# Kernel tuning notes

Hardware: AMD Instinct MI355X
Metric: run time of the kernel (lower is better)

The kernel has to match this reference:

```python
import jax, jax.numpy as jnp
import numpy as np

EPS = 1e-06
N_HEADS = 8


def setup_inputs() -> dict:
    key = jax.random.key(0)
    ks = jax.random.split(key, 9)
    B, M, T, C = 2, 64, 256, 512
    s = 0.02
    return {
        "x": jax.random.normal(ks[0], (B, M, T, C), dtype=jnp.float32),
        "Wq": jax.random.normal(ks[1], (C, C), dtype=jnp.float32) * s,
        "bq": jnp.zeros((C,), dtype=jnp.float32),
        "Wk": jax.random.normal(ks[2], (C, C), dtype=jnp.float32) * s,
        "bk": jnp.zeros((C,), dtype=jnp.float32),
        "Wv": jax.random.normal(ks[3], (C, C), dtype=jnp.float32) * s,
        "bv": jnp.zeros((C,), dtype=jnp.float32),
        "Wp": jax.random.normal(ks[4], (C, C), dtype=jnp.float32) * s,
        "bp": jnp.zeros((C,), dtype=jnp.float32),
    }


def _proj_heads(x, W, b, N, D):
    # nn.Linear: x @ W.T + b, then view(B,M,T,N,D).transpose(2,3) -> [B,M,N,T,D]
    B, M, T, C = x.shape
    y = jnp.einsum('bmtc,dc->bmtd', x, W) + b
    return y.reshape(B, M, T, N, D).transpose(0, 1, 3, 2, 4)


def reference(x, Wq, bq, Wk, bk, Wv, bv, Wp, bp):
    B, M, T, C = x.shape
    N = N_HEADS
    D = C // N
    q = _proj_heads(x, Wq, bq, N, D)  # [B,M,N,T,D]
    k = _proj_heads(x, Wk, bk, N, D)
    v = _proj_heads(x, Wv, bv, N, D)
    # ELU+1 feature map
    q = jax.nn.elu(q) + 1.0
    k = jax.nn.elu(k) + 1.0
    # KtV = k^T @ v : [B,M,N,D,D]
    KtV = jnp.einsum('bmntd,bmnte->bmnde', k, v)
    # Z = 1 / (q @ sum_t k + eps) : [B,M,N,T]
    ksum = jnp.sum(k, axis=-2)  # [B,M,N,D]
    z = 1.0 / (jnp.einsum('bmntd,bmnd->bmnt', q, ksum) + EPS)
    # Original does Z.expand(...,D) @ KtV; since Z is constant over the D axis,
    # this equals z[t] * sum_d KtV[d, e] -- compute that directly (faithful math).
    KtV_colsum = jnp.sum(KtV, axis=-2)  # [B,M,N,D]
    V = z[..., None] * KtV_colsum[..., None, :]  # [B,M,N,T,D]
    V = V.transpose(0, 1, 3, 2, 4).reshape(B, M, T, N * D)
    out = jnp.einsum('bmtc,dc->bmtd', V, Wp) + bp
    return out
```

## Files before the change

### kernel.cpp

```cpp
#include <hip/hip_runtime.h>
#include <hip/hip_bf16.h>

#define BM_ 128
#define T_  256
#define C_  512
#define NH  8
#define DH  64

typedef __bf16 bf16;
typedef __attribute__((ext_vector_type(8))) __bf16 bf16x8;
typedef __attribute__((ext_vector_type(4))) float f32x4;

__device__ __forceinline__ float elu1(float v){ return v > 0.f ? v + 1.f : __expf(v); }

__device__ __forceinline__ unsigned short f2bf(float f){
  unsigned u = __float_as_uint(f);
  u += 0x7fffu + ((u >> 16) & 1u);
  return (unsigned short)(u >> 16);
}

__device__ __forceinline__ float bf2f(unsigned short b){
  return __uint_as_float(((unsigned)b) << 16);
}

#define GLOAD16(gptr, lptr) __builtin_amdgcn_global_load_lds( \
  (const __attribute__((address_space(1))) void*)(gptr), \
  (__attribute__((address_space(3))) void*)(lptr), 16, 0, 0)

__global__ __launch_bounds__(256) void cvt3_kernel(
    const float* __restrict__ a, int na4,
    const float* __restrict__ b, int nb4,
    const float* __restrict__ c, int nc4,
    unsigned short* __restrict__ oa, unsigned short* __restrict__ ob,
    unsigned short* __restrict__ oc)
{
  int i = blockIdx.x * blockDim.x + threadIdx.x;
  int stride = gridDim.x * blockDim.x;
  int total = na4 + nb4 + nc4;
  for (; i < total; i += stride) {
    const float* src; unsigned short* dst; int idx;
    if (i < na4)            { src = a; dst = oa; idx = i; }
    else if (i < na4 + nb4) { src = b; dst = ob; idx = i - na4; }
    else                    { src = c; dst = oc; idx = i - na4 - nb4; }
    float4 v = reinterpret_cast<const float4*>(src)[idx];
    ushort4 o;
    o.x = f2bf(v.x); o.y = f2bf(v.y); o.z = f2bf(v.z); o.w = f2bf(v.w);
    reinterpret_cast<ushort4*>(dst)[idx] = o;
  }
}

template<int MODE>
__global__ __launch_bounds__(256) void gemm_proj(
    const bf16* __restrict__ A, const bf16* __restrict__ Bw,
    const float* __restrict__ bias,
    float* __restrict__ krow, float* __restrict__ ksum4,
    const float* __restrict__ ksum4_in, float* __restrict__ zden)
{
  __shared__ bf16 As[2][128 * 32];
  __shared__ bf16 Bs[2][128 * 32];

  const int tid  = threadIdx.x;
  const int lane = tid & 63;
  const int wid  = tid >> 6;
  const int wm   = wid >> 1, wn = wid & 1;

  const int L  = (blockIdx.x & 7) * 128 + (blockIdx.x >> 3);
  const int tn = L & 3, tm = L >> 2;

  f32x4 acc[4][4];
#pragma unroll
  for (int i = 0; i < 4; i++)
#pragma unroll
    for (int j = 0; j < 4; j++) acc[i][j] = (f32x4){0.f, 0.f, 0.f, 0.f};

  const bf16* Ab = A  + (size_t)(tm * 128) * C_;
  const bf16* Bb = Bw + (size_t)(tn * 128) * C_;

  const int r0 = tid >> 2, r1 = r0 + 64;
  const int sl = (tid & 3) * 8;
  const int fr = lane & 15;
  const int fq = lane >> 4;
  const int fk = fq * 8;

#define STAGE(buf, kc) do { \
    GLOAD16(Ab + (size_t)r0 * C_ + (kc) + sl, As[buf] + r0 * 32 + sl); \
    GLOAD16(Ab + (size_t)r1 * C_ + (kc) + sl, As[buf] + r1 * 32 + sl); \
    GLOAD16(Bb + (size_t)r0 * C_ + (kc) + sl, Bs[buf] + r0 * 32 + sl); \
    GLOAD16(Bb + (size_t)r1 * C_ + (kc) + sl, Bs[buf] + r1 * 32 + sl); \
  } while (0)

  STAGE(0, 0);
  asm volatile("s_waitcnt vmcnt(0)" ::: "memory");
  __syncthreads();

  for (int it = 0; it < 15; ++it) {
    const int cur = it & 1;
    STAGE(cur ^ 1, (it + 1) * 32);
    bf16x8 af[4], bfr[4];
#pragma unroll
    for (int i = 0; i < 4; i++)
      af[i] = *reinterpret_cast<const bf16x8*>(&As[cur][(wm * 64 + i * 16 + fr) * 32 + fk]);
#pragma unroll
    for (int j = 0; j < 4; j++)
      bfr[j] = *reinterpret_cast<const bf16x8*>(&Bs[cur][(wn * 64 + j * 16 + fr) * 32 + fk]);
#pragma unroll
    for (int i = 0; i < 4; i++)
#pragma unroll
      for (int j = 0; j < 4; j++)
        acc[i][j] = __builtin_amdgcn_mfma_f32_16x16x32_bf16(af[i], bfr[j], acc[i][j], 0, 0, 0);
    asm volatile("s_waitcnt vmcnt(0)" ::: "memory");
    __syncthreads();
  }
  {
    bf16x8 af[4], bfr[4];
#pragma unroll
    for (int i = 0; i < 4; i++)
      af[i] = *reinterpret_cast<const bf16x8*>(&As[1][(wm * 64 + i * 16 + fr) * 32 + fk]);
#pragma unroll
    for (int j = 0; j < 4; j++)
      bfr[j] = *reinterpret_cast<const bf16x8*>(&Bs[1][(wn * 64 + j * 16 + fr) * 32 + fk]);
#pragma unroll
    for (int i = 0; i < 4; i++)
#pragma unroll
      for (int j = 0; j < 4; j++)
        acc[i][j] = __builtin_amdgcn_mfma_f32_16x16x32_bf16(af[i], bfr[j], acc[i][j], 0, 0, 0);
  }
#undef STAGE

  const int bm   = tm >> 1;
  const int head = tn * 2 + wn;
  float bj[4];
#pragma unroll
  for (int j = 0; j < 4; j++) bj[j] = bias[tn * 128 + wn * 64 + j * 16 + fr];

  if (MODE == 0) {
    float cs[4] = {0.f, 0.f, 0.f, 0.f};
#pragma unroll
    for (int i = 0; i < 4; i++) {
#pragma unroll
      for (int r = 0; r < 4; r++) {
        float rs = 0.f;
#pragma unroll
        for (int j = 0; j < 4; j++) {
          float v = elu1(acc[i][j][r] + bj[j]);
          rs += v;
          cs[j] += v;
        }
#pragma unroll
        for (int m = 1; m < 16; m <<= 1) rs += __shfl_xor(rs, m);
        if (fr == 0) {
          int grow = tm * 128 + wm * 64 + i * 16 + fq * 4 + r;
          krow[((size_t)bm * NH + head) * T_ + (grow & 255)] = rs;
        }
      }
    }
    const int part = (tm & 1) * 2 + wm;
#pragma unroll
    for (int j = 0; j < 4; j++) {
      cs[j] += __shfl_xor(cs[j], 16);
      cs[j] += __shfl_xor(cs[j], 32);
      if (fq == 0)
        ksum4[((size_t)part * BM_ + bm) * C_ + tn * 128 + wn * 64 + j * 16 + fr] = cs[j];
    }
  } else {
    float ks[4];
#pragma unroll
    for (int j = 0; j < 4; j++) {
      size_t col = (size_t)bm * C_ + tn * 128 + wn * 64 + j * 16 + fr;
      ks[j] = ksum4_in[col] + ksum4_in[(size_t)BM_ * C_ + col]
            + ksum4_in[2 * (size_t)BM_ * C_ + col] + ksum4_in[3 * (size_t)BM_ * C_ + col];
    }
#pragma unroll
    for (int i = 0; i < 4; i++) {
#pragma unroll
      for (int r = 0; r < 4; r++) {
        float zs = 0.f;
#pragma unroll
        for (int j = 0; j < 4; j++) zs = fmaf(elu1(acc[i][j][r] + bj[j]), ks[j], zs);
#pragma unroll
        for (int m = 1; m < 16; m <<= 1) zs += __shfl_xor(zs, m);
        if (fr == 0) {
          int grow = tm * 128 + wm * 64 + i * 16 + fq * 4 + r;
          zden[((size_t)bm * NH + head) * T_ + (grow & 255)] = zs;
        }
      }
    }
  }
}

__global__ __launch_bounds__(256) void xk_kernel(
    const unsigned short* __restrict__ xb, const float* __restrict__ krow,
    float* __restrict__ xk2, float* __restrict__ srow2)
{
  const int bm = blockIdx.x, th = blockIdx.y, tid = threadIdx.x;
  __shared__ float krs[NH * 128];
#pragma unroll
  for (int p = 0; p < 4; p++) {
    int idx = tid + p * 256;
    int n = idx >> 7, t = idx & 127;
    krs[idx] = krow[((size_t)bm * NH + n) * T_ + th * 128 + t];
  }
  __syncthreads();
  float a0[8], a1[8];
#pragma unroll
  for (int n = 0; n < 8; n++) { a0[n] = 0.f; a1[n] = 0.f; }
  const unsigned short* xp = xb + ((size_t)bm * T_ + th * 128) * C_ + tid * 2;
  for (int t = 0; t < 128; t++) {
    ushort2 u = *reinterpret_cast<const ushort2*>(xp + (size_t)t * C_);
    float x0 = bf2f(u.x), x1 = bf2f(u.y);
#pragma unroll
    for (int n = 0; n < 8; n++) {
      float kr = krs[n * 128 + t];
      a0[n] = fmaf(kr, x0, a0[n]);
      a1[n] = fmaf(kr, x1, a1[n]);
    }
  }
#pragma unroll
  for (int n = 0; n < 8; n++)
    *reinterpret_cast<float2*>(&xk2[(((size_t)th * BM_ + bm) * NH + n) * C_ + tid * 2])
        = make_float2(a0[n], a1[n]);
  if (tid < 8) {
    float s = 0.f;
    for (int t = 0; t < 128; t++) s += krs[tid * 128 + t];
    srow2[((size_t)th * BM_ + bm) * NH + tid] = s;
  }
}

__global__ __launch_bounds__(256) void colsum_kernel(
    const float* __restrict__ xk2, const float* __restrict__ srow2,
    const float* __restrict__ Wv, const float* __restrict__ bv,
    float* __restrict__ cs_g)
{
  const int bm0 = blockIdx.x * 8, h = blockIdx.y, tid = threadIdx.x;
  __shared__ float4 xs4[8][128];
#pragma unroll
  for (int p = 0; p < 4; p++) {
    int idx = tid + p * 256;
    int bmr = idx >> 7, c4 = idx & 127;
    float4 u = *reinterpret_cast<const float4*>(
        xk2 + (((size_t)0 * BM_ + bm0 + bmr) * NH + h) * C_ + c4 * 4);
    float4 w = *reinterpret_cast<const float4*>(
        xk2 + (((size_t)1 * BM_ + bm0 + bmr) * NH + h) * C_ + c4 * 4);
    xs4[bmr][c4] = make_float4(u.x + w.x, u.y + w.y, u.z + w.z, u.w + w.w);
  }
  __syncthreads();
  const int e = tid & 63, bs = tid >> 6;
  const float4* wv4 = reinterpret_cast<const float4*>(Wv + (size_t)(h * DH + e) * C_);
  float acc0 = 0.f, acc1 = 0.f;
#pragma unroll 4
  for (int c4 = 0; c4 < 128; c4++) {
    float4 w = wv4[c4];
    float4 a = xs4[bs * 2][c4];
    float4 b = xs4[bs * 2 + 1][c4];
    acc0 += w.x * a.x + w.y * a.y + w.z * a.z + w.w * a.w;
    acc1 += w.x * b.x + w.y * b.y + w.z * b.z + w.w * b.w;
  }
  float bve = bv[h * DH + e];
  int bmA = bm0 + bs * 2, bmB = bmA + 1;
  float sA = srow2[(size_t)bmA * NH + h] + srow2[(size_t)(BM_ + bmA) * NH + h];
  float sB = srow2[(size_t)bmB * NH + h] + srow2[(size_t)(BM_ + bmB) * NH + h];
  cs_g[((size_t)bmA * NH + h) * DH + e] = acc0 + sA * bve;
  cs_g[((size_t)bmB * NH + h) * DH + e] = acc1 + sB * bve;
}

__global__ __launch_bounds__(256) void wbuf_kernel(
    const float* __restrict__ cs_g, const float* __restrict__ Wp,
    float* __restrict__ wbuf)
{
  const int cpt = blockIdx.x, h = blockIdx.y, bm0 = blockIdx.z * 16;
  const int tid = threadIdx.x;
  __shared__ float4 csL4[16][16];
  {
    int bmr = tid >> 4, e4 = tid & 15;
    csL4[bmr][e4] = *reinterpret_cast<const float4*>(
        cs_g + ((size_t)(bm0 + bmr) * NH + h) * DH + e4 * 4);
  }
  __syncthreads();
  const int cp = cpt * 256 + tid;
  float4 wp[16];
  const float4* wpr = reinterpret_cast<const float4*>(Wp + (size_t)cp * C_ + h * DH);
#pragma unroll
  for (int e4 = 0; e4 < 16; e4++) wp[e4] = wpr[e4];
#pragma unroll
  for (int bmr = 0; bmr < 16; bmr++) {
    float acc = 0.f;
#pragma unroll
    for (int e4 = 0; e4 < 16; e4++) {
      float4 c = csL4[bmr][e4];
      acc += wp[e4].x * c.x + wp[e4].y * c.y + wp[e4].z * c.z + wp[e4].w * c.w;
    }
    wbuf[((size_t)(bm0 + bmr) * NH + h) * C_ + cp] = acc;
  }
}

__global__ __launch_bounds__(256) void out_kernel(
    const float* __restrict__ zden, const float* __restrict__ wbuf,
    const float* __restrict__ bp, float* __restrict__ out)
{
  const int bm = blockIdx.x, tt = blockIdx.y, tid = threadIdx.x;
  __shared__ float zs[NH][64];
#pragma unroll
  for (int p = 0; p < 2; p++) {
    int idx = tid + p * 256;
    int n = idx >> 6, t = idx & 63;
    zs[n][t] = 1.f / (zden[((size_t)bm * NH + n) * T_ + tt * 64 + t] + 1e-6f);
  }
  float2 wv[8];
  const int c2 = tid * 2;
#pragma unroll
  for (int n = 0; n < 8; n++)
    wv[n] = *reinterpret_cast<const float2*>(wbuf + ((size_t)bm * NH + n) * C_ + c2);
  float2 bpv = *reinterpret_cast<const float2*>(bp + c2);
  __syncthreads();
  float* ob = out + ((size_t)bm * T_ + tt * 64) * C_;
  for (int t = 0; t < 64; t++) {
    float o0 = bpv.x, o1 = bpv.y;
#pragma unroll
    for (int n = 0; n < 8; n++) { float z = zs[n][t]; o0 = fmaf(z, wv[n].x, o0); o1 = fmaf(z, wv[n].y, o1); }
    *reinterpret_cast<float2*>(ob + (size_t)t * C_ + c2) = make_float2(o0, o1);
  }
}

extern "C" void kernel_launch(void* const* d_in, const int* in_sizes, int n_in,
                              void* d_out, int out_size, void* d_ws, size_t ws_size,
                              hipStream_t stream)
{
  const float* x  = (const float*)d_in[0];
  const float* Wq = (const float*)d_in[1];
  const float* bq = (const float*)d_in[2];
  const float* Wk = (const float*)d_in[3];
  const float* bk = (const float*)d_in[4];
  const float* Wv = (const float*)d_in[5];
  const float* bv = (const float*)d_in[6];
  const float* Wp = (const float*)d_in[7];
  const float* bp = (const float*)d_in[8];
  float* out = (float*)d_out;

  float* ws    = (float*)d_ws;
  float* zden  = ws;
  float* ksum4 = zden + 262144;
  float* krow  = ksum4 + 262144;
  float* srow2 = krow + 262144;
  float* xk2   = srow2 + 2048;
  float* cs    = xk2 + 1048576;
  float* wbuf  = cs + 65536;
  unsigned short* xb  = (unsigned short*)(wbuf + 524288);
  unsigned short* wkb = xb + 16777216;
  unsigned short* wqb = wkb + 262144;

  cvt3_kernel<<<2048, 256, 0, stream>>>(x, 16777216 / 4, Wk, 262144 / 4, Wq, 262144 / 4,
                                        xb, wkb, wqb);

  gemm_proj<0><<<1024, 256, 0, stream>>>((const bf16*)xb, (const bf16*)wkb, bk,
                                         krow, ksum4, nullptr, nullptr);
  xk_kernel<<<dim3(BM_, 2), 256, 0, stream>>>(xb, krow, xk2, srow2);
  colsum_kernel<<<dim3(16, 8), 256, 0, stream>>>(xk2, srow2, Wv, bv, cs);
  wbuf_kernel<<<dim3(2, 8, 8), 256, 0, stream>>>(cs, Wp, wbuf);
  gemm_proj<1><<<1024, 256, 0, stream>>>((const bf16*)xb, (const bf16*)wqb, bq,
                                         nullptr, nullptr, ksum4, zden);
  out_kernel<<<dim3(BM_, 4), 256, 0, stream>>>(zden, wbuf, bp, out);
}
```

Before: 135.6 us.

## Enlarge projection GEMM tiles to 256x256 with swizzled LDS and interleaved prefetch

Rewrites the bf16 projection GEMM to use 256x256 block tiles with K=64 steps, 512 threads (8 waves), an XOR-swizzled LDS layout, and prefetch of the next K tile split into chunks between quarter-step MFMA groups, with s_setprio around the MFMA bursts. Larger tiles cut the number of times A and B are re-read from global memory, and the swizzle is meant to avoid LDS bank conflicts. The xk reduction is also split across four T-quarters instead of two to add parallelism. The cost is 128KB of LDS per block and a heavy register footprint, which limits occupancy. The grid also shrinks to 256 blocks, which may leave some CUs unevenly loaded.

```diff
diff --git a/kernel.cpp b/kernel.cpp
--- a/kernel.cpp
+++ b/kernel.cpp
@@ -26,6 +26,8 @@
 #define GLOAD16(gptr, lptr) __builtin_amdgcn_global_load_lds( \
   (const __attribute__((address_space(1))) void*)(gptr), \
   (__attribute__((address_space(3))) void*)(lptr), 16, 0, 0)
+
+#define FENCE() asm volatile("" ::: "memory")
 
 __global__ __launch_bounds__(256) void cvt3_kernel(
     const float* __restrict__ a, int na4,
@@ -50,138 +52,190 @@
 }
 
 template<int MODE>
-__global__ __launch_bounds__(256) void gemm_proj(
+__global__ __launch_bounds__(512, 2) void gemm_proj(
     const bf16* __restrict__ A, const bf16* __restrict__ Bw,
     const float* __restrict__ bias,
-    float* __restrict__ krow, float* __restrict__ ksum4,
-    const float* __restrict__ ksum4_in, float* __restrict__ zden)
-{
-  __shared__ bf16 As[2][128 * 32];
-  __shared__ bf16 Bs[2][128 * 32];
+    float* __restrict__ krow, float* __restrict__ ksum2,
+    const float* __restrict__ ksum2_in, float* __restrict__ zden)
+{
+  __shared__ bf16 As[2][256 * 64];
+  __shared__ bf16 Bs[2][256 * 64];
 
   const int tid  = threadIdx.x;
   const int lane = tid & 63;
   const int wid  = tid >> 6;
-  const int wm   = wid >> 1, wn = wid & 1;
-
-  const int L  = (blockIdx.x & 7) * 128 + (blockIdx.x >> 3);
-  const int tn = L & 3, tm = L >> 2;
-
-  f32x4 acc[4][4];
-#pragma unroll
-  for (int i = 0; i < 4; i++)
-#pragma unroll
-    for (int j = 0; j < 4; j++) acc[i][j] = (f32x4){0.f, 0.f, 0.f, 0.f};
-
-  const bf16* Ab = A  + (size_t)(tm * 128) * C_;
-  const bf16* Bb = Bw + (size_t)(tn * 128) * C_;
-
-  const int r0 = tid >> 2, r1 = r0 + 64;
-  const int sl = (tid & 3) * 8;
-  const int fr = lane & 15;
-  const int fq = lane >> 4;
-  const int fk = fq * 8;
-
-#define STAGE(buf, kc) do { \
-    GLOAD16(Ab + (size_t)r0 * C_ + (kc) + sl, As[buf] + r0 * 32 + sl); \
-    GLOAD16(Ab + (size_t)r1 * C_ + (kc) + sl, As[buf] + r1 * 32 + sl); \
-    GLOAD16(Bb + (size_t)r0 * C_ + (kc) + sl, Bs[buf] + r0 * 32 + sl); \
-    GLOAD16(Bb + (size_t)r1 * C_ + (kc) + sl, Bs[buf] + r1 * 32 + sl); \
-  } while (0)
-
-  STAGE(0, 0);
+  const int wr   = wid >> 2, wc = wid & 3;
+
+  const int L  = ((blockIdx.x & 7) << 5) + (blockIdx.x >> 3);
+  const int tn = L & 1, tm = L >> 1;
+
+  const bf16* Ab = A  + (size_t)(tm * 256) * C_;
+  const bf16* Bb = Bw + (size_t)(tn * 256) * C_;
+
+  const int srow  = tid >> 3;
+  const int sslot = tid & 7;
+  const int fr = lane & 15, fq = lane >> 4;
+
+  f32x4 acc[8][4];
+#pragma unroll
+  for (int m = 0; m < 8; ++m)
+#pragma unroll
+    for (int n = 0; n < 4; ++n) acc[m][n] = (f32x4){0.f, 0.f, 0.f, 0.f};
+
+#define STG(XS, Xb, b, h, kt) do { \
+  _Pragma("unroll") \
+  for (int q = 0; q < 2; ++q) { \
+    int r_ = (h) * 128 + q * 64 + srow; \
+    GLOAD16(Xb + (size_t)r_ * C_ + (kt) * 64 + ((sslot ^ (r_ & 7)) << 3), \
+            &XS[b][(((h) * 128 + q * 64) << 6) + (tid << 3)]); \
+  } } while (0)
+
+#define LOFF(row, sl) (((row) << 6) + ((((sl) ^ ((row) & 7))) << 3))
+
+  STG(As, Ab, 0, 0, 0); STG(As, Ab, 0, 1, 0);
+  STG(Bs, Bb, 0, 0, 0); STG(Bs, Bb, 0, 1, 0);
   asm volatile("s_waitcnt vmcnt(0)" ::: "memory");
-  __syncthreads();
-
-  for (int it = 0; it < 15; ++it) {
-    const int cur = it & 1;
-    STAGE(cur ^ 1, (it + 1) * 32);
-    bf16x8 af[4], bfr[4];
-#pragma unroll
-    for (int i = 0; i < 4; i++)
-      af[i] = *reinterpret_cast<const bf16x8*>(&As[cur][(wm * 64 + i * 16 + fr) * 32 + fk]);
-#pragma unroll
-    for (int j = 0; j < 4; j++)
-      bfr[j] = *reinterpret_cast<const bf16x8*>(&Bs[cur][(wn * 64 + j * 16 + fr) * 32 + fk]);
-#pragma unroll
-    for (int i = 0; i < 4; i++)
-#pragma unroll
-      for (int j = 0; j < 4; j++)
-        acc[i][j] = __builtin_amdgcn_mfma_f32_16x16x32_bf16(af[i], bfr[j], acc[i][j], 0, 0, 0);
+  __builtin_amdgcn_s_barrier();
+  FENCE();
+
+  bf16x8 af[4][2], bfr[4][2];
+
+  for (int t = 0; t < 8; ++t) {
+    const int cur = t & 1;
+    const bool pre = (t < 7);
+#pragma unroll
+    for (int m = 0; m < 4; ++m)
+#pragma unroll
+      for (int kk = 0; kk < 2; ++kk) {
+        int row = wr * 128 + m * 16 + fr;
+        af[m][kk] = *reinterpret_cast<const bf16x8*>(&As[cur][LOFF(row, kk * 4 + fq)]);
+      }
+#pragma unroll
+    for (int n = 0; n < 2; ++n)
+#pragma unroll
+      for (int kk = 0; kk < 2; ++kk) {
+        int row = wc * 64 + n * 16 + fr;
+        bfr[n][kk] = *reinterpret_cast<const bf16x8*>(&Bs[cur][LOFF(row, kk * 4 + fq)]);
+      }
+    if (pre) { STG(As, Ab, cur ^ 1, 0, t + 1); STG(Bs, Bb, cur ^ 1, 0, t + 1); }
+    __builtin_amdgcn_s_setprio(1);
+#pragma unroll
+    for (int m = 0; m < 4; ++m)
+#pragma unroll
+      for (int n = 0; n < 2; ++n)
+#pragma unroll
+        for (int kk = 0; kk < 2; ++kk)
+          acc[m][n] = __builtin_amdgcn_mfma_f32_16x16x32_bf16(af[m][kk], bfr[n][kk], acc[m][n], 0, 0, 0);
+    __builtin_amdgcn_s_setprio(0);
+    __builtin_amdgcn_s_barrier();
+    FENCE();
+#pragma unroll
+    for (int n = 0; n < 2; ++n)
+#pragma unroll
+      for (int kk = 0; kk < 2; ++kk) {
+        int row = wc * 64 + (n + 2) * 16 + fr;
+        bfr[n + 2][kk] = *reinterpret_cast<const bf16x8*>(&Bs[cur][LOFF(row, kk * 4 + fq)]);
+      }
+    if (pre) STG(As, Ab, cur ^ 1, 1, t + 1);
+    __builtin_amdgcn_s_setprio(1);
+#pragma unroll
+    for (int m = 0; m < 4; ++m)
+#pragma unroll
+      for (int n = 0; n < 2; ++n)
+#pragma unroll
+        for (int kk = 0; kk < 2; ++kk)
+          acc[m][n + 2] = __builtin_amdgcn_mfma_f32_16x16x32_bf16(af[m][kk], bfr[n + 2][kk], acc[m][n + 2], 0, 0, 0);
+    __builtin_amdgcn_s_setprio(0);
+    __builtin_amdgcn_s_barrier();
+    FENCE();
+#pragma unroll
+    for (int m = 0; m < 4; ++m)
+#pragma unroll
+      for (int kk = 0; kk < 2; ++kk) {
+        int row = wr * 128 + 64 + m * 16 + fr;
+        af[m][kk] = *reinterpret_cast<const bf16x8*>(&As[cur][LOFF(row, kk * 4 + fq)]);
+      }
+    if (pre) STG(Bs, Bb, cur ^ 1, 1, t + 1);
+    __builtin_amdgcn_s_setprio(1);
+#pragma unroll
+    for (int m = 0; m < 4; ++m)
+#pragma unroll
+      for (int n = 0; n < 2; ++n)
+#pragma unroll
+        for (int kk = 0; kk < 2; ++kk)
+          acc[m + 4][n] = __builtin_amdgcn_mfma_f32_16x16x32_bf16(af[m][kk], bfr[n][kk], acc[m + 4][n], 0, 0, 0);
+    __builtin_amdgcn_s_setprio(0);
+    __builtin_amdgcn_s_barrier();
+    FENCE();
+    __builtin_amdgcn_s_setprio(1);
+#pragma unroll
+    for (int m = 0; m < 4; ++m)
+#pragma unroll
+      for (int n = 0; n < 2; ++n)
+#pragma unroll
+        for (int kk = 0; kk < 2; ++kk)
+          acc[m + 4][n + 2] = __builtin_amdgcn_mfma_f32_16x16x32_bf16(af[m][kk], bfr[n + 2][kk], acc[m + 4][n + 2], 0, 0, 0);
+    __builtin_amdgcn_s_setprio(0);
     asm volatile("s_waitcnt vmcnt(0)" ::: "memory");
-    __syncthreads();
-  }
-  {
-    bf16x8 af[4], bfr[4];
-#pragma unroll
-    for (int i = 0; i < 4; i++)
-      af[i] = *reinterpret_cast<const bf16x8*>(&As[1][(wm * 64 + i * 16 + fr) * 32 + fk]);
-#pragma unroll
-    for (int j = 0; j < 4; j++)
-      bfr[j] = *reinterpret_cast<const bf16x8*>(&Bs[1][(wn * 64 + j * 16 + fr) * 32 + fk]);
-#pragma unroll
-    for (int i = 0; i < 4; i++)
-#pragma unroll
-      for (int j = 0; j < 4; j++)
-        acc[i][j] = __builtin_amdgcn_mfma_f32_16x16x32_bf16(af[i], bfr[j], acc[i][j], 0, 0, 0);
-  }
-#undef STAGE
-
-  const int bm   = tm >> 1;
-  const int head = tn * 2 + wn;
+    __builtin_amdgcn_s_barrier();
+    FENCE();
+  }
+#undef STG
+#undef LOFF
+
+  const int bm   = tm;
+  const int head = tn * 4 + wc;
   float bj[4];
 #pragma unroll
-  for (int j = 0; j < 4; j++) bj[j] = bias[tn * 128 + wn * 64 + j * 16 + fr];
+  for (int n = 0; n < 4; ++n) bj[n] = bias[tn * 256 + wc * 64 + n * 16 + fr];
 
   if (MODE == 0) {
     float cs[4] = {0.f, 0.f, 0.f, 0.f};
 #pragma unroll
-    for (int i = 0; i < 4; i++) {
-#pragma unroll
-      for (int r = 0; r < 4; r++) {
+    for (int m = 0; m < 8; ++m) {
+#pragma unroll
+      for (int r = 0; r < 4; ++r) {
         float rs = 0.f;
 #pragma unroll
-        for (int j = 0; j < 4; j++) {
-          float v = elu1(acc[i][j][r] + bj[j]);
+        for (int n = 0; n < 4; ++n) {
+          float v = elu1(acc[m][n][r] + bj[n]);
           rs += v;
-          cs[j] += v;
+          cs[n] += v;
         }
 #pragma unroll
-        for (int m = 1; m < 16; m <<= 1) rs += __shfl_xor(rs, m);
+        for (int msk = 1; msk < 16; msk <<= 1) rs += __shfl_xor(rs, msk);
         if (fr == 0) {
-          int grow = tm * 128 + wm * 64 + i * 16 + fq * 4 + r;
-          krow[((size_t)bm * NH + head) * T_ + (grow & 255)] = rs;
+          int tg = wr * 128 + m * 16 + fq * 4 + r;
+          krow[((size_t)bm * NH + head) * T_ + tg] = rs;
         }
       }
     }
-    const int part = (tm & 1) * 2 + wm;
-#pragma unroll
-    for (int j = 0; j < 4; j++) {
-      cs[j] += __shfl_xor(cs[j], 16);
-      cs[j] += __shfl_xor(cs[j], 32);
+#pragma unroll
+    for (int n = 0; n < 4; ++n) {
+      cs[n] += __shfl_xor(cs[n], 16);
+      cs[n] += __shfl_xor(cs[n], 32);
       if (fq == 0)
-        ksum4[((size_t)part * BM_ + bm) * C_ + tn * 128 + wn * 64 + j * 16 + fr] = cs[j];
+        ksum2[((size_t)wr * BM_ + bm) * C_ + tn * 256 + wc * 64 + n * 16 + fr] = cs[n];
     }
   } else {
     float ks[4];
 #pragma unroll
-    for (int j = 0; j < 4; j++) {
-      size_t col = (size_t)bm * C_ + tn * 128 + wn * 64 + j * 16 + fr;
-      ks[j] = ksum4_in[col] + ksum4_in[(size_t)BM_ * C_ + col]
-            + ksum4_in[2 * (size_t)BM_ * C_ + col] + ksum4_in[3 * (size_t)BM_ * C_ + col];
-    }
-#pragma unroll
-    for (int i = 0; i < 4; i++) {
-#pragma unroll
-      for (int r = 0; r < 4; r++) {
+    for (int n = 0; n < 4; ++n) {
+      size_t col = (size_t)bm * C_ + tn * 256 + wc * 64 + n * 16 + fr;
+      ks[n] = ksum2_in[col] + ksum2_in[(size_t)BM_ * C_ + col];
+    }
+#pragma unroll
+    for (int m = 0; m < 8; ++m) {
+#pragma unroll
+      for (int r = 0; r < 4; ++r) {
         float zs = 0.f;
 #pragma unroll
-        for (int j = 0; j < 4; j++) zs = fmaf(elu1(acc[i][j][r] + bj[j]), ks[j], zs);
-#pragma unroll
-        for (int m = 1; m < 16; m <<= 1) zs += __shfl_xor(zs, m);
+        for (int n = 0; n < 4; ++n) zs = fmaf(elu1(acc[m][n][r] + bj[n]), ks[n], zs);
+#pragma unroll
+        for (int msk = 1; msk < 16; msk <<= 1) zs += __shfl_xor(zs, msk);
         if (fr == 0) {
-          int grow = tm * 128 + wm * 64 + i * 16 + fq * 4 + r;
-          zden[((size_t)bm * NH + head) * T_ + (grow & 255)] = zs;
+          int tg = wr * 128 + m * 16 + fq * 4 + r;
+          zden[((size_t)bm * NH + head) * T_ + tg] = zs;
         }
       }
     }
@@ -190,65 +244,68 @@
 
 __global__ __launch_bounds__(256) void xk_kernel(
     const unsigned short* __restrict__ xb, const float* __restrict__ krow,
-    float* __restrict__ xk2, float* __restrict__ srow2)
-{
-  const int bm = blockIdx.x, th = blockIdx.y, tid = threadIdx.x;
-  __shared__ float krs[NH * 128];
-#pragma unroll
-  for (int p = 0; p < 4; p++) {
+    float* __restrict__ xk4, float* __restrict__ srow4)
+{
+  const int bm = blockIdx.x, qt = blockIdx.y, tid = threadIdx.x;
+  __shared__ float krs[NH * 64];
+#pragma unroll
+  for (int p = 0; p < 2; ++p) {
     int idx = tid + p * 256;
-    int n = idx >> 7, t = idx & 127;
-    krs[idx] = krow[((size_t)bm * NH + n) * T_ + th * 128 + t];
+    int n = idx >> 6, t = idx & 63;
+    krs[idx] = krow[((size_t)bm * NH + n) * T_ + qt * 64 + t];
   }
   __syncthreads();
   float a0[8], a1[8];
 #pragma unroll
-  for (int n = 0; n < 8; n++) { a0[n] = 0.f; a1[n] = 0.f; }
-  const unsigned short* xp = xb + ((size_t)bm * T_ + th * 128) * C_ + tid * 2;
-  for (int t = 0; t < 128; t++) {
+  for (int n = 0; n < 8; ++n) { a0[n] = 0.f; a1[n] = 0.f; }
+  const unsigned short* xp = xb + ((size_t)bm * T_ + qt * 64) * C_ + tid * 2;
+  for (int t = 0; t < 64; ++t) {
     ushort2 u = *reinterpret_cast<const ushort2*>(xp + (size_t)t * C_);
     float x0 = bf2f(u.x), x1 = bf2f(u.y);
 #pragma unroll
-    for (int n = 0; n < 8; n++) {
-      float kr = krs[n * 128 + t];
+    for (int n = 0; n < 8; ++n) {
+      float kr = krs[n * 64 + t];
       a0[n] = fmaf(kr, x0, a0[n]);
       a1[n] = fmaf(kr, x1, a1[n]);
     }
   }
 #pragma unroll
-  for (int n = 0; n < 8; n++)
-    *reinterpret_cast<float2*>(&xk2[(((size_t)th * BM_ + bm) * NH + n) * C_ + tid * 2])
+  for (int n = 0; n < 8; ++n)
+    *reinterpret_cast<float2*>(&xk4[(((size_t)qt * BM_ + bm) * NH + n) * C_ + tid * 2])
         = make_float2(a0[n], a1[n]);
   if (tid < 8) {
     float s = 0.f;
-    for (int t = 0; t < 128; t++) s += krs[tid * 128 + t];
-    srow2[((size_t)th * BM_ + bm) * NH + tid] = s;
+    for (int t = 0; t < 64; ++t) s += krs[tid * 64 + t];
+    srow4[((size_t)qt * BM_ + bm) * NH + tid] = s;
   }
 }
 
 __global__ __launch_bounds__(256) void colsum_kernel(
-    const float* __restrict__ xk2, const float* __restrict__ srow2,
+    const float* __restrict__ xk4, const float* __restrict__ srow4,
     const float* __restrict__ Wv, const float* __restrict__ bv,
     float* __restrict__ cs_g)
 {
   const int bm0 = blockIdx.x * 8, h = blockIdx.y, tid = threadIdx.x;
   __shared__ float4 xs4[8][128];
 #pragma unroll
-  for (int p = 0; p < 4; p++) {
+  for (int p = 0; p < 4; ++p) {
     int idx = tid + p * 256;
     int bmr = idx >> 7, c4 = idx & 127;
-    float4 u = *reinterpret_cast<const float4*>(
-        xk2 + (((size_t)0 * BM_ + bm0 + bmr) * NH + h) * C_ + c4 * 4);
-    float4 w = *reinterpret_cast<const float4*>(
-        xk2 + (((size_t)1 * BM_ + bm0 + bmr) * NH + h) * C_ + c4 * 4);
-    xs4[bmr][c4] = make_float4(u.x + w.x, u.y + w.y, u.z + w.z, u.w + w.w);
+    float4 s = make_float4(0.f, 0.f, 0.f, 0.f);
+#pragma unroll
+    for (int q = 0; q < 4; ++q) {
+      float4 u = *reinterpret_cast<const float4*>(
+          xk4 + (((size_t)q * BM_ + bm0 + bmr) * NH + h) * C_ + c4 * 4);
+      s.x += u.x; s.y += u.y; s.z += u.z; s.w += u.w;
+    }
+    xs4[bmr][c4] = s;
   }
   __syncthreads();
   const int e = tid & 63, bs = tid >> 6;
   const float4* wv4 = reinterpret_cast<const float4*>(Wv + (size_t)(h * DH + e) * C_);
   float acc0 = 0.f, acc1 = 0.f;
 #pragma unroll 4
-  for (int c4 = 0; c4 < 128; c4++) {
+  for (int c4 = 0; c4 < 128; ++c4) {
     float4 w = wv4[c4];
     float4 a = xs4[bs * 2][c4];
     float4 b = xs4[bs * 2 + 1][c4];
@@ -257,8 +314,12 @@
   }
   float bve = bv[h * DH + e];
   int bmA = bm0 + bs * 2, bmB = bmA + 1;
-  float sA = srow2[(size_t)bmA * NH + h] + srow2[(size_t)(BM_ + bmA) * NH + h];
-  float sB = srow2[(size_t)bmB * NH + h] + srow2[(size_t)(BM_ + bmB) * NH + h];
+  float sA = 0.f, sB = 0.f;
+#pragma unroll
+  for (int q = 0; q < 4; ++q) {
+    sA += srow4[((size_t)q * BM_ + bmA) * NH + h];
+    sB += srow4[((size_t)q * BM_ + bmB) * NH + h];
+  }
   cs_g[((size_t)bmA * NH + h) * DH + e] = acc0 + sA * bve;
   cs_g[((size_t)bmB * NH + h) * DH + e] = acc1 + sB * bve;
 }
@@ -280,12 +341,12 @@
   float4 wp[16];
   const float4* wpr = reinterpret_cast<const float4*>(Wp + (size_t)cp * C_ + h * DH);
 #pragma unroll
-  for (int e4 = 0; e4 < 16; e4++) wp[e4] = wpr[e4];
-#pragma unroll
-  for (int bmr = 0; bmr < 16; bmr++) {
+  for (int e4 = 0; e4 < 16; ++e4) wp[e4] = wpr[e4];
+#pragma unroll
+  for (int bmr = 0; bmr < 16; ++bmr) {
     float acc = 0.f;
 #pragma unroll
-    for (int e4 = 0; e4 < 16; e4++) {
+    for (int e4 = 0; e4 < 16; ++e4) {
       float4 c = csL4[bmr][e4];
       acc += wp[e4].x * c.x + wp[e4].y * c.y + wp[e4].z * c.z + wp[e4].w * c.w;
     }
@@ -300,7 +361,7 @@
   const int bm = blockIdx.x, tt = blockIdx.y, tid = threadIdx.x;
   __shared__ float zs[NH][64];
 #pragma unroll
-  for (int p = 0; p < 2; p++) {
+  for (int p = 0; p < 2; ++p) {
     int idx = tid + p * 256;
     int n = idx >> 6, t = idx & 63;
     zs[n][t] = 1.f / (zden[((size_t)bm * NH + n) * T_ + tt * 64 + t] + 1e-6f);
@@ -308,15 +369,15 @@
   float2 wv[8];
   const int c2 = tid * 2;
 #pragma unroll
-  for (int n = 0; n < 8; n++)
+  for (int n = 0; n < 8; ++n)
     wv[n] = *reinterpret_cast<const float2*>(wbuf + ((size_t)bm * NH + n) * C_ + c2);
   float2 bpv = *reinterpret_cast<const float2*>(bp + c2);
   __syncthreads();
   float* ob = out + ((size_t)bm * T_ + tt * 64) * C_;
-  for (int t = 0; t < 64; t++) {
+  for (int t = 0; t < 64; ++t) {
     float o0 = bpv.x, o1 = bpv.y;
 #pragma unroll
-    for (int n = 0; n < 8; n++) { float z = zs[n][t]; o0 = fmaf(z, wv[n].x, o0); o1 = fmaf(z, wv[n].y, o1); }
+    for (int n = 0; n < 8; ++n) { float z = zs[n][t]; o0 = fmaf(z, wv[n].x, o0); o1 = fmaf(z, wv[n].y, o1); }
     *reinterpret_cast<float2*>(ob + (size_t)t * C_ + c2) = make_float2(o0, o1);
   }
 }
@@ -338,11 +399,11 @@
 
   float* ws    = (float*)d_ws;
   float* zden  = ws;
-  float* ksum4 = zden + 262144;
-  float* krow  = ksum4 + 262144;
-  float* srow2 = krow + 262144;
-  float* xk2   = srow2 + 2048;
-  float* cs    = xk2 + 1048576;
+  float* ksum2 = zden + 262144;
+  float* krow  = ksum2 + 131072;
+  float* srow4 = krow + 262144;
+  float* xk4   = srow4 + 4096;
+  float* cs    = xk4 + 2097152;
   float* wbuf  = cs + 65536;
   unsigned short* xb  = (unsigned short*)(wbuf + 524288);
   unsigned short* wkb = xb + 16777216;
@@ -351,12 +412,12 @@
   cvt3_kernel<<<2048, 256, 0, stream>>>(x, 16777216 / 4, Wk, 262144 / 4, Wq, 262144 / 4,
                                         xb, wkb, wqb);
 
-  gemm_proj<0><<<1024, 256, 0, stream>>>((const bf16*)xb, (const bf16*)wkb, bk,
-                                         krow, ksum4, nullptr, nullptr);
-  xk_kernel<<<dim3(BM_, 2), 256, 0, stream>>>(xb, krow, xk2, srow2);
-  colsum_kernel<<<dim3(16, 8), 256, 0, stream>>>(xk2, srow2, Wv, bv, cs);
+  gemm_proj<0><<<256, 512, 0, stream>>>((const bf16*)xb, (const bf16*)wkb, bk,
+                                        krow, ksum2, nullptr, nullptr);
+  xk_kernel<<<dim3(BM_, 4), 256, 0, stream>>>(xb, krow, xk4, srow4);
+  colsum_kernel<<<dim3(16, 8), 256, 0, stream>>>(xk4, srow4, Wv, bv, cs);
   wbuf_kernel<<<dim3(2, 8, 8), 256, 0, stream>>>(cs, Wp, wbuf);
-  gemm_proj<1><<<1024, 256, 0, stream>>>((const bf16*)xb, (const bf16*)wqb, bq,
-                                         nullptr, nullptr, ksum4, zden);
+  gemm_proj<1><<<256, 512, 0, stream>>>((const bf16*)xb, (const bf16*)wqb, bq,
+                                        nullptr, nullptr, ksum2, zden);
   out_kernel<<<dim3(BM_, 4), 256, 0, stream>>>(zden, wbuf, bp, out);
 }
```

Measured after the change: 115.9 us. 14.5% less time.
